# Optimization experiments

Measured on AMD Instinct MI355X. Metric: run time of the kernel, lower is better.

Reference implementation:

```python
import jax, jax.numpy as jnp
import numpy as np

N_NODES = 100000
N_EDGES = 1600000
IN_C, HID_C, OUT_C = 64, 64, 32


def setup_inputs() -> dict:
    key = jax.random.key(0)
    ks = jax.random.split(key, 6)
    x = jax.random.normal(ks[0], (N_NODES, IN_C), dtype=jnp.float32)
    edge_index = jax.random.randint(ks[1], (2, N_EDGES), 0, N_NODES, dtype=jnp.int64)
    edge_weight = jax.random.uniform(ks[2], (N_EDGES,), dtype=jnp.float32)
    # Glorot-ish init for the two GCNConv weight matrices, zero bias (PyG default)
    W1 = jax.random.normal(ks[3], (IN_C, HID_C), dtype=jnp.float32) / np.sqrt(IN_C)
    b1 = jnp.zeros((HID_C,), dtype=jnp.float32)
    W2 = jax.random.normal(ks[4], (HID_C, OUT_C), dtype=jnp.float32) / np.sqrt(HID_C)
    b2 = jnp.zeros((OUT_C,), dtype=jnp.float32)
    return {"x": x, "edge_index": edge_index, "edge_weight": edge_weight,
            "W1": W1, "b1": b1, "W2": W2, "b2": b2}


def _gcn_conv(x, src, dst, w, W, b):
    """PyG GCNConv: add self-loops (weight 1), symmetric D^-1/2 (A+I) D^-1/2 norm,
    then aggregate transformed features into destination nodes, plus bias."""
    n = x.shape[0]
    loop = jnp.arange(n, dtype=src.dtype)
    s = jnp.concatenate([src, loop])
    d = jnp.concatenate([dst, loop])
    wl = jnp.concatenate([w, jnp.ones((n,), dtype=x.dtype)])
    deg = jax.ops.segment_sum(wl, d, num_segments=n)            # [N]
    dinv = jnp.where(deg > 0, jax.lax.rsqrt(deg), 0.0)
    norm = dinv[s] * wl * dinv[d]                               # [E+N]
    xw = x @ W                                                  # [N, C_out]
    msg = norm[:, None] * xw[s]                                 # gather + scale
    return jax.ops.segment_sum(msg, d, num_segments=n) + b      # scatter-add


def reference(x, edge_index, edge_weight, W1, b1, W2, b2):
    src, dst = edge_index[0], edge_index[1]
    h = _gcn_conv(x, src, dst, edge_weight, W1, b1)
    h = jax.nn.relu(h)
    # dropout(p=0.5, training=self.training): identity in eval mode
    return _gcn_conv(h, src, dst, edge_weight, W2, b2)
```

## Files before the change

kernel.cpp:

```cpp
#include <hip/hip_runtime.h>

#define N_NODES 100000
#define N_EDGES 1600000
#define IN_C 64
#define HID_C 64
#define OUT_C 32

#define NB 391
#define BSHIFT 8
#define BMASK 255
#define SEG_CAP 4864
#define EPB 4096
#define BIN_BLOCKS ((N_EDGES + EPB - 1) / EPB)
#define G1_BLOCKS ((N_NODES + 63) / 64)
#define SMASK 0x1FFFF
#define FIXSCALE 34359738368.0f

__device__ __forceinline__ unsigned int bpack(float a, float b) {
    unsigned int ua = __float_as_uint(a);
    ua += 0x7FFFu + ((ua >> 16) & 1u);
    unsigned int ub = __float_as_uint(b);
    ub += 0x7FFFu + ((ub >> 16) & 1u);
    return (ua >> 16) | (ub & 0xFFFF0000u);
}
__device__ __forceinline__ float2 bup(unsigned int v) {
    return make_float2(__uint_as_float(v << 16), __uint_as_float(v & 0xFFFF0000u));
}


struct BinSh {
    int meta[EPB];
    int hist[NB];
    int gbase[NB];
};
struct G1Sh {
    float XsT[64][64];
    float Ws[64][64];
};
union FusedSh { BinSh b; G1Sh g; };

__global__ void __launch_bounds__(256) fused1_kernel(
    const int* __restrict__ src, const int* __restrict__ dst,
    const float* __restrict__ w, int* __restrict__ gcnt, int2* __restrict__ seg,
    const float* __restrict__ X, const float* __restrict__ W,
    unsigned int* __restrict__ XWu) {
    __shared__ FusedSh sh;
    int tid = threadIdx.x;
    if (blockIdx.x < BIN_BLOCKS) {
        for (int i = tid; i < NB; i += 256) sh.b.hist[i] = 0;
        __syncthreads();
        int e0 = blockIdx.x * EPB;
        int n = min(EPB, N_EDGES - e0);
        const int4* dst4 = (const int4*)(dst + e0);
        int n4 = n >> 2;
        for (int i = tid; i < n4; i += 256) {
            int4 d = dst4[i];
            int b0 = d.x >> BSHIFT, b1 = d.y >> BSHIFT;
            int b2 = d.z >> BSHIFT, b3 = d.w >> BSHIFT;
            sh.b.meta[0 * n4 + i] = atomicAdd(&sh.b.hist[b0], 1);
            sh.b.meta[1 * n4 + i] = atomicAdd(&sh.b.hist[b1], 1);
            sh.b.meta[2 * n4 + i] = atomicAdd(&sh.b.hist[b2], 1);
            sh.b.meta[3 * n4 + i] = atomicAdd(&sh.b.hist[b3], 1);
        }
        __syncthreads();
        for (int b = tid; b < NB; b += 256) {
            int c = sh.b.hist[b];
            sh.b.gbase[b] = c ? atomicAdd(&gcnt[b], c) : 0;
        }
        __syncthreads();
        const int4* src4 = (const int4*)(src + e0);
        const float4* w4 = (const float4*)(w + e0);
        for (int i = tid; i < n4; i += 256) {
            int4 s = src4[i];
            int4 d = dst4[i];
            float4 ww = w4[i];
#define FL_ONE(K, SS, DD, WW)                                              \
            {                                                              \
                int b = (DD) >> BSHIFT;                                    \
                int pos = sh.b.gbase[b] + sh.b.meta[K * n4 + i];           \
                if (pos < SEG_CAP)                                         \
                    seg[(size_t)b * SEG_CAP + pos] =                       \
                        make_int2((SS) | (((DD) & BMASK) << 17),           \
                                  __float_as_int(WW));                     \
            }
            FL_ONE(0, s.x, d.x, ww.x)
            FL_ONE(1, s.y, d.y, ww.y)
            FL_ONE(2, s.z, d.z, ww.z)
            FL_ONE(3, s.w, d.w, ww.w)
#undef FL_ONE
        }
    } else {
        {
            const float4* Wv = (const float4*)W;
            float4* Wsv = (float4*)&sh.g.Ws[0][0];
            for (int i = tid; i < 1024; i += 256) Wsv[i] = Wv[i];
        }
        int row0 = (blockIdx.x - BIN_BLOCKS) * 64;
        int rmax = N_NODES - row0;
        for (int i = tid; i < 64 * 16; i += 256) {
            int r = i & 63, kq = i >> 6;
            float4 v = (r < rmax) ? ((const float4*)(X + (size_t)(row0 + r) * IN_C))[kq]
                                  : make_float4(0.f, 0.f, 0.f, 0.f);
            sh.g.XsT[4 * kq + 0][r] = v.x;
            sh.g.XsT[4 * kq + 1][r] = v.y;
            sh.g.XsT[4 * kq + 2][r] = v.z;
            sh.g.XsT[4 * kq + 3][r] = v.w;
        }
        __syncthreads();
        int tr = tid >> 4, tc = tid & 15;
        float acc[4][4] = {};
        float a[4], bb[4];
#pragma unroll 8
        for (int k = 0; k < 64; ++k) {
            *(float4*)a = *(const float4*)&sh.g.XsT[k][4 * tr];
            *(float4*)bb = *(const float4*)&sh.g.Ws[k][4 * tc];
#pragma unroll
            for (int i = 0; i < 4; ++i)
#pragma unroll
                for (int j = 0; j < 4; ++j) acc[i][j] += a[i] * bb[j];
        }
#pragma unroll
        for (int i = 0; i < 4; ++i) {
            int rl = 4 * tr + i;
            if (rl < rmax) {
                int row = row0 + rl;
                uint2 o;
                o.x = bpack(acc[i][0], acc[i][1]);
                o.y = bpack(acc[i][2], acc[i][3]);
                ((uint2*)XWu)[(size_t)row * 16 + tc] = o;
            }
        }
    }
}


__global__ void __launch_bounds__(1024) bsort_kernel(const int* __restrict__ gcnt,
                                                     const int2* __restrict__ seg,
                                                     int2* __restrict__ seg2,
                                                     float* __restrict__ dinv,
                                                     int2* __restrict__ rowRC,
                                                     unsigned int* __restrict__ XWs) {
    __shared__ unsigned long long packed[256];
    __shared__ int meta[SEG_CAP];
    __shared__ int sarr[256];
    __shared__ int ofs0[256];
    __shared__ float dinvsh[256];
    int tid = threadIdx.x, b = blockIdx.x;
    int n = min(gcnt[b], SEG_CAP);
    const int2* sp = seg + (size_t)b * SEG_CAP;
    if (tid < 256) packed[tid] = 0ULL;
    __syncthreads();
    for (int i = tid; i < n; i += 1024) {
        int2 r = sp[i];
        int dl = (r.x >> 17) & BMASK;
        unsigned long long fixw =
            (unsigned long long)(__int_as_float(r.y) * FIXSCALE);
        unsigned long long old = atomicAdd(&packed[dl], (1ULL << 48) | fixw);
        meta[i] = dl | ((int)(old >> 48) << 8);
    }
    __syncthreads();
    int myc = 0, padc = 0;
    if (tid < 256) {
        unsigned long long p = packed[tid];
        myc = (int)(p >> 48);
        float degw = (float)((double)(p & ((1ULL << 48) - 1)) * (1.0 / (double)FIXSCALE));
        float dv = rsqrtf(1.0f + degw);
        dinvsh[tid] = dv;
        int node = (b << BSHIFT) + tid;
        if (node < N_NODES) dinv[node] = dv;
        padc = (myc + 1) & ~1;
        sarr[tid] = padc;
    }
    __syncthreads();
    for (int off = 1; off < 256; off <<= 1) {
        int tmp = 0;
        if (tid < 256 && tid >= off) tmp = sarr[tid - off];
        __syncthreads();
        if (tid < 256) sarr[tid] += tmp;
        __syncthreads();
    }
    if (tid < 256) {
        int excl = sarr[tid] - padc;
        int node = (b << BSHIFT) + tid;
        if (node < N_NODES) rowRC[node] = make_int2(b * SEG_CAP + excl, myc);
        ofs0[tid] = excl;
    }
    __syncthreads();
    int2* op = seg2 + (size_t)b * SEG_CAP;
    for (int i = tid; i < n; i += 1024) {
        int2 r = sp[i];
        int m = meta[i];
        int dl = m & BMASK, rank = m >> 8;
        op[ofs0[dl] + rank] = r;
    }
    int baseRow = b << BSHIFT;
    int rowsHere = min(256, N_NODES - baseRow);
    uint4* XW4 = (uint4*)XWs;
    for (int i = tid; i < rowsHere * 8; i += 1024) {
        int nl = i >> 3;
        float s = dinvsh[nl];
        uint4 v = XW4[(size_t)(baseRow + nl) * 8 + (i & 7)];
        float2 f;
        f = bup(v.x); v.x = bpack(f.x * s, f.y * s);
        f = bup(v.y); v.y = bpack(f.x * s, f.y * s);
        f = bup(v.z); v.z = bpack(f.x * s, f.y * s);
        f = bup(v.w); v.w = bpack(f.x * s, f.y * s);
        XW4[(size_t)(baseRow + nl) * 8 + (i & 7)] = v;
    }
}


__global__ void __launch_bounds__(256) agg1_kernel(const int2* __restrict__ rowRC,
                                                   const int2* __restrict__ seg2,
                                                   const unsigned int* __restrict__ XWs,
                                                   const float* __restrict__ dinv,
                                                   const float* __restrict__ b1,
                                                   unsigned int* __restrict__ Hb) {
    int l16 = threadIdx.x & 15;
    int d = blockIdx.x * 16 + (threadIdx.x >> 4);
    if (d >= N_NODES) return;
    const uint2* XW2 = (const uint2*)XWs;
    float did = dinv[d];
    float4 bv = ((const float4*)b1)[l16];
    uint2 sv = XW2[(size_t)d * 16 + l16];
    float2 f0 = bup(sv.x), f1 = bup(sv.y);
    float a0 = bv.x + did * f0.x, a1 = bv.y + did * f0.y;
    float a2 = bv.z + did * f1.x, a3 = bv.w + did * f1.y;
    int2 rc = rowRC[d];
    int nc = rc.y;
    const int2* sp = seg2 + rc.x;
    const int4* sp4 = (const int4*)sp;
    int e = 0;
    for (; e + 8 <= nc; e += 8) {
        int4 q0 = sp4[(e >> 1) + 0], q1 = sp4[(e >> 1) + 1];
        int4 q2 = sp4[(e >> 1) + 2], q3 = sp4[(e >> 1) + 3];
        int s0 = q0.x & SMASK, s1 = q0.z & SMASK, s2 = q1.x & SMASK, s3 = q1.z & SMASK;
        int s4 = q2.x & SMASK, s5 = q2.z & SMASK, s6 = q3.x & SMASK, s7 = q3.z & SMASK;
        uint2 r0 = XW2[(size_t)s0 * 16 + l16];
        uint2 r1 = XW2[(size_t)s1 * 16 + l16];
        uint2 r2 = XW2[(size_t)s2 * 16 + l16];
        uint2 r3 = XW2[(size_t)s3 * 16 + l16];
        uint2 r4 = XW2[(size_t)s4 * 16 + l16];
        uint2 r5 = XW2[(size_t)s5 * 16 + l16];
        uint2 r6 = XW2[(size_t)s6 * 16 + l16];
        uint2 r7 = XW2[(size_t)s7 * 16 + l16];
        float c0 = __int_as_float(q0.y) * did, c1 = __int_as_float(q0.w) * did;
        float c2 = __int_as_float(q1.y) * did, c3 = __int_as_float(q1.w) * did;
        float c4 = __int_as_float(q2.y) * did, c5 = __int_as_float(q2.w) * did;
        float c6 = __int_as_float(q3.y) * did, c7 = __int_as_float(q3.w) * did;
        float2 v;
#define ACC1(R, C)                                                         \
        v = bup(R.x); a0 += (C) * v.x; a1 += (C) * v.y;                    \
        v = bup(R.y); a2 += (C) * v.x; a3 += (C) * v.y;
        ACC1(r0, c0) ACC1(r1, c1) ACC1(r2, c2) ACC1(r3, c3)
        ACC1(r4, c4) ACC1(r5, c5) ACC1(r6, c6) ACC1(r7, c7)
    }
    for (; e + 2 <= nc; e += 2) {
        int4 q = sp4[e >> 1];
        int s0 = q.x & SMASK, s1 = q.z & SMASK;
        uint2 r0 = XW2[(size_t)s0 * 16 + l16];
        uint2 r1 = XW2[(size_t)s1 * 16 + l16];
        float c0 = __int_as_float(q.y) * did, c1 = __int_as_float(q.w) * did;
        float2 v;
        ACC1(r0, c0) ACC1(r1, c1)
    }
    if (e < nc) {
        int2 p = sp[e];
        int s = p.x & SMASK;
        float c = __int_as_float(p.y) * did;
        uint2 r = XW2[(size_t)s * 16 + l16];
        float2 v;
        ACC1(r, c)
    }
#undef ACC1
    uint2 o;
    o.x = bpack(fmaxf(a0, 0.f), fmaxf(a1, 0.f));
    o.y = bpack(fmaxf(a2, 0.f), fmaxf(a3, 0.f));
    ((uint2*)Hb)[(size_t)d * 16 + l16] = o;
}


__global__ void __launch_bounds__(256) gemm2_kernel(const unsigned int* __restrict__ Hb,
                                                    const float* __restrict__ W,
                                                    const float* __restrict__ dinv,
                                                    unsigned int* __restrict__ HWs,
                                                    int nRows) {
    __shared__ float HsT[64][128];
    __shared__ float Ws[64][32];
    int tid = threadIdx.x;
    {
        const float4* Wv = (const float4*)W;
        float4* Wsv = (float4*)&Ws[0][0];
        for (int i = tid; i < 512; i += 256) Wsv[i] = Wv[i];
    }
    int row0 = blockIdx.x * 128;
    int rmax = nRows - row0;
    for (int i = tid; i < 128 * 8; i += 256) {
        int r = i & 127, kq = i >> 7;
        uint4 v = (r < rmax) ? ((const uint4*)(Hb + (size_t)(row0 + r) * 32))[kq]
                             : make_uint4(0u, 0u, 0u, 0u);
        float2 f;
        f = bup(v.x); HsT[8 * kq + 0][r] = f.x; HsT[8 * kq + 1][r] = f.y;
        f = bup(v.y); HsT[8 * kq + 2][r] = f.x; HsT[8 * kq + 3][r] = f.y;
        f = bup(v.z); HsT[8 * kq + 4][r] = f.x; HsT[8 * kq + 5][r] = f.y;
        f = bup(v.w); HsT[8 * kq + 6][r] = f.x; HsT[8 * kq + 7][r] = f.y;
    }
    __syncthreads();
    int tr = tid >> 3, tc = tid & 7;
    float acc[4][4] = {};
    float a[4], bb[4];
#pragma unroll 8
    for (int k = 0; k < 64; ++k) {
        *(float4*)a = *(const float4*)&HsT[k][4 * tr];
        *(float4*)bb = *(const float4*)&Ws[k][4 * tc];
#pragma unroll
        for (int i = 0; i < 4; ++i)
#pragma unroll
            for (int j = 0; j < 4; ++j) acc[i][j] += a[i] * bb[j];
    }
#pragma unroll
    for (int i = 0; i < 4; ++i) {
        int rl = 4 * tr + i;
        if (rl < rmax) {
            int row = row0 + rl;
            float di = dinv[row];
            uint2 o;
            o.x = bpack(acc[i][0] * di, acc[i][1] * di);
            o.y = bpack(acc[i][2] * di, acc[i][3] * di);
            ((uint2*)HWs)[(size_t)row * 8 + tc] = o;
        }
    }
}


__global__ void __launch_bounds__(256) agg2_kernel(const int2* __restrict__ rowRC,
                                                   const int2* __restrict__ seg2,
                                                   const unsigned int* __restrict__ HWs,
                                                   const float* __restrict__ dinv,
                                                   const float* __restrict__ b2,
                                                   float* __restrict__ out) {
    int l8 = threadIdx.x & 7;
    int d = blockIdx.x * 32 + (threadIdx.x >> 3);
    if (d >= N_NODES) return;
    const uint2* HW2 = (const uint2*)HWs;
    float did = dinv[d];
    float4 bv = ((const float4*)b2)[l8];
    uint2 sv = HW2[(size_t)d * 8 + l8];
    float2 f0 = bup(sv.x), f1 = bup(sv.y);
    float a0 = bv.x + did * f0.x, a1 = bv.y + did * f0.y;
    float a2 = bv.z + did * f1.x, a3 = bv.w + did * f1.y;
    int2 rc = rowRC[d];
    int nc = rc.y;
    const int2* sp = seg2 + rc.x;
    const int4* sp4 = (const int4*)sp;
    int e = 0;
    for (; e + 8 <= nc; e += 8) {
        int4 q0 = sp4[(e >> 1) + 0], q1 = sp4[(e >> 1) + 1];
        int4 q2 = sp4[(e >> 1) + 2], q3 = sp4[(e >> 1) + 3];
        int s0 = q0.x & SMASK, s1 = q0.z & SMASK, s2 = q1.x & SMASK, s3 = q1.z & SMASK;
        int s4 = q2.x & SMASK, s5 = q2.z & SMASK, s6 = q3.x & SMASK, s7 = q3.z & SMASK;
        uint2 r0 = HW2[(size_t)s0 * 8 + l8];
        uint2 r1 = HW2[(size_t)s1 * 8 + l8];
        uint2 r2 = HW2[(size_t)s2 * 8 + l8];
        uint2 r3 = HW2[(size_t)s3 * 8 + l8];
        uint2 r4 = HW2[(size_t)s4 * 8 + l8];
        uint2 r5 = HW2[(size_t)s5 * 8 + l8];
        uint2 r6 = HW2[(size_t)s6 * 8 + l8];
        uint2 r7 = HW2[(size_t)s7 * 8 + l8];
        float c0 = __int_as_float(q0.y) * did, c1 = __int_as_float(q0.w) * did;
        float c2 = __int_as_float(q1.y) * did, c3 = __int_as_float(q1.w) * did;
        float c4 = __int_as_float(q2.y) * did, c5 = __int_as_float(q2.w) * did;
        float c6 = __int_as_float(q3.y) * did, c7 = __int_as_float(q3.w) * did;
        float2 v;
#define ACC2(R, C)                                                         \
        v = bup(R.x); a0 += (C) * v.x; a1 += (C) * v.y;                    \
        v = bup(R.y); a2 += (C) * v.x; a3 += (C) * v.y;
        ACC2(r0, c0) ACC2(r1, c1) ACC2(r2, c2) ACC2(r3, c3)
        ACC2(r4, c4) ACC2(r5, c5) ACC2(r6, c6) ACC2(r7, c7)
    }
    for (; e + 2 <= nc; e += 2) {
        int4 q = sp4[e >> 1];
        int s0 = q.x & SMASK, s1 = q.z & SMASK;
        uint2 r0 = HW2[(size_t)s0 * 8 + l8];
        uint2 r1 = HW2[(size_t)s1 * 8 + l8];
        float c0 = __int_as_float(q.y) * did, c1 = __int_as_float(q.w) * did;
        float2 v;
        ACC2(r0, c0) ACC2(r1, c1)
    }
    if (e < nc) {
        int2 p = sp[e];
        int s = p.x & SMASK;
        float c = __int_as_float(p.y) * did;
        uint2 r = HW2[(size_t)s * 8 + l8];
        float2 v;
        ACC2(r, c)
    }
#undef ACC2
    ((float4*)out)[(size_t)d * 8 + l8] = make_float4(a0, a1, a2, a3);
}


extern "C" void kernel_launch(void* const* d_in, const int* in_sizes, int n_in,
                              void* d_out, int out_size, void* d_ws, size_t ws_size,
                              hipStream_t stream) {
    const float* x = (const float*)d_in[0];
    const int* edge_index = (const int*)d_in[1];
    const float* ew = (const float*)d_in[2];
    const float* W1 = (const float*)d_in[3];
    const float* b1 = (const float*)d_in[4];
    const float* W2 = (const float*)d_in[5];
    const float* b2 = (const float*)d_in[6];
    float* out = (float*)d_out;

    const int* src = edge_index;
    const int* dst = edge_index + N_EDGES;

    char* ws = (char*)d_ws;
    size_t off = 0;
    auto carve = [&](size_t bytes) -> void* {
        void* p = ws + off;
        off += (bytes + 255) & ~(size_t)255;
        return p;
    };

    int* gcnt = (int*)carve(NB * 4);
    float* dinv = (float*)carve((size_t)N_NODES * 4);
    int2* rowRC = (int2*)carve((size_t)N_NODES * 8);
    int2* seg = (int2*)carve((size_t)NB * SEG_CAP * 8);
    int2* seg2 = (int2*)carve((size_t)NB * SEG_CAP * 8);
    unsigned int* XWs = (unsigned int*)carve((size_t)N_NODES * 32 * 4);
    unsigned int* Hb = (unsigned int*)carve((size_t)N_NODES * 32 * 4);
    unsigned int* HWs = XWs;

    hipMemsetAsync(gcnt, 0, NB * 4, stream);
    fused1_kernel<<<BIN_BLOCKS + G1_BLOCKS, 256, 0, stream>>>(src, dst, ew, gcnt, seg,
                                                              x, W1, XWs);
    bsort_kernel<<<NB, 1024, 0, stream>>>(gcnt, seg, seg2, dinv, rowRC, XWs);
    agg1_kernel<<<(N_NODES + 15) / 16, 256, 0, stream>>>(rowRC, seg2, XWs, dinv, b1, Hb);
    gemm2_kernel<<<(N_NODES + 127) / 128, 256, 0, stream>>>(Hb, W2, dinv, HWs, N_NODES);
    agg2_kernel<<<(N_NODES + 31) / 32, 256, 0, stream>>>(rowRC, seg2, HWs, dinv, b2, out);
}
```

Measured before the change: 217.9 us.

## Fuse second-layer GEMM into first aggregation kernel via shared memory

The first aggregation kernel now stages each block's 16 ReLU'd hidden rows in shared memory and multiplies them by W2, loaded into LDS, writing the dinv-scaled bf16 HW rows directly. This drops the separate gemm2 kernel and the bf16 H buffer write and read round trip, plus one launch. In exchange, agg1 uses more LDS and a __syncthreads, the early-exit bound check is removed (this relies on N_NODES being divisible by 16), and each thread does a 64-step dot product with less register reuse than the tiled GEMM.

```diff
diff --git a/kernel.cpp b/kernel.cpp
--- a/kernel.cpp
+++ b/kernel.cpp
@@ -215,10 +215,19 @@
                                                    const unsigned int* __restrict__ XWs,
                                                    const float* __restrict__ dinv,
                                                    const float* __restrict__ b1,
-                                                   unsigned int* __restrict__ Hb) {
-    int l16 = threadIdx.x & 15;
-    int d = blockIdx.x * 16 + (threadIdx.x >> 4);
-    if (d >= N_NODES) return;
+                                                   const float* __restrict__ W2,
+                                                   unsigned int* __restrict__ HWs) {
+    __shared__ float Hs[16][68];
+    __shared__ float Ws2[64][32];
+    int tid = threadIdx.x;
+    {
+        const float4* Wv = (const float4*)W2;
+        float4* Wsv = (float4*)&Ws2[0][0];
+        for (int i = tid; i < 512; i += 256) Wsv[i] = Wv[i];
+    }
+    int l16 = tid & 15;
+    int nl = tid >> 4;
+    int d = blockIdx.x * 16 + nl;
     const uint2* XW2 = (const uint2*)XWs;
     float did = dinv[d];
     float4 bv = ((const float4*)b1)[l16];
@@ -273,63 +282,19 @@
         ACC1(r, c)
     }
 #undef ACC1
-    uint2 o;
-    o.x = bpack(fmaxf(a0, 0.f), fmaxf(a1, 0.f));
-    o.y = bpack(fmaxf(a2, 0.f), fmaxf(a3, 0.f));
-    ((uint2*)Hb)[(size_t)d * 16 + l16] = o;
-}
-
-
-__global__ void __launch_bounds__(256) gemm2_kernel(const unsigned int* __restrict__ Hb,
-                                                    const float* __restrict__ W,
-                                                    const float* __restrict__ dinv,
-                                                    unsigned int* __restrict__ HWs,
-                                                    int nRows) {
-    __shared__ float HsT[64][128];
-    __shared__ float Ws[64][32];
-    int tid = threadIdx.x;
-    {
-        const float4* Wv = (const float4*)W;
-        float4* Wsv = (float4*)&Ws[0][0];
-        for (int i = tid; i < 512; i += 256) Wsv[i] = Wv[i];
-    }
-    int row0 = blockIdx.x * 128;
-    int rmax = nRows - row0;
-    for (int i = tid; i < 128 * 8; i += 256) {
-        int r = i & 127, kq = i >> 7;
-        uint4 v = (r < rmax) ? ((const uint4*)(Hb + (size_t)(row0 + r) * 32))[kq]
-                             : make_uint4(0u, 0u, 0u, 0u);
-        float2 f;
-        f = bup(v.x); HsT[8 * kq + 0][r] = f.x; HsT[8 * kq + 1][r] = f.y;
-        f = bup(v.y); HsT[8 * kq + 2][r] = f.x; HsT[8 * kq + 3][r] = f.y;
-        f = bup(v.z); HsT[8 * kq + 4][r] = f.x; HsT[8 * kq + 5][r] = f.y;
-        f = bup(v.w); HsT[8 * kq + 6][r] = f.x; HsT[8 * kq + 7][r] = f.y;
-    }
+    *(float4*)&Hs[nl][4 * l16] = make_float4(fmaxf(a0, 0.f), fmaxf(a1, 0.f),
+                                             fmaxf(a2, 0.f), fmaxf(a3, 0.f));
     __syncthreads();
-    int tr = tid >> 3, tc = tid & 7;
-    float acc[4][4] = {};
-    float a[4], bb[4];
-#pragma unroll 8
+    int c0i = l16 * 2;
+    float o0 = 0.f, o1 = 0.f;
+#pragma unroll
     for (int k = 0; k < 64; ++k) {
-        *(float4*)a = *(const float4*)&HsT[k][4 * tr];
-        *(float4*)bb = *(const float4*)&Ws[k][4 * tc];
-#pragma unroll
-        for (int i = 0; i < 4; ++i)
-#pragma unroll
-            for (int j = 0; j < 4; ++j) acc[i][j] += a[i] * bb[j];
-    }
-#pragma unroll
-    for (int i = 0; i < 4; ++i) {
-        int rl = 4 * tr + i;
-        if (rl < rmax) {
-            int row = row0 + rl;
-            float di = dinv[row];
-            uint2 o;
-            o.x = bpack(acc[i][0] * di, acc[i][1] * di);
-            o.y = bpack(acc[i][2] * di, acc[i][3] * di);
-            ((uint2*)HWs)[(size_t)row * 8 + tc] = o;
-        }
-    }
+        float hk = Hs[nl][k];
+        float2 wv = *(const float2*)&Ws2[k][c0i];
+        o0 += hk * wv.x;
+        o1 += hk * wv.y;
+    }
+    ((unsigned int*)HWs)[(size_t)d * 16 + l16] = bpack(o0 * did, o1 * did);
 }
 
 
@@ -429,14 +394,12 @@
     int2* seg = (int2*)carve((size_t)NB * SEG_CAP * 8);
     int2* seg2 = (int2*)carve((size_t)NB * SEG_CAP * 8);
     unsigned int* XWs = (unsigned int*)carve((size_t)N_NODES * 32 * 4);
-    unsigned int* Hb = (unsigned int*)carve((size_t)N_NODES * 32 * 4);
-    unsigned int* HWs = XWs;
+    unsigned int* HWs = (unsigned int*)carve((size_t)N_NODES * 16 * 4);
 
     hipMemsetAsync(gcnt, 0, NB * 4, stream);
     fused1_kernel<<<BIN_BLOCKS + G1_BLOCKS, 256, 0, stream>>>(src, dst, ew, gcnt, seg,
                                                               x, W1, XWs);
     bsort_kernel<<<NB, 1024, 0, stream>>>(gcnt, seg, seg2, dinv, rowRC, XWs);
-    agg1_kernel<<<(N_NODES + 15) / 16, 256, 0, stream>>>(rowRC, seg2, XWs, dinv, b1, Hb);
-    gemm2_kernel<<<(N_NODES + 127) / 128, 256, 0, stream>>>(Hb, W2, dinv, HWs, N_NODES);
+    agg1_kernel<<<N_NODES / 16, 256, 0, stream>>>(rowRC, seg2, XWs, dinv, b1, W2, HWs);
     agg2_kernel<<<(N_NODES + 31) / 32, 256, 0, stream>>>(rowRC, seg2, HWs, dinv, b2, out);
 }
```

After: 207.2 us. 4.9% less time.
